# Kernel optimization log

Hardware: AMD Instinct MI355X
Metric: run time of the kernel (lower is better)

Reference implementation:

```python
import jax, jax.numpy as jnp
import numpy as np

PIXEL_THRESHOLD = 0.4
FRACTION_THRESHOLD = 0.03
NUM_CLASSES = 20
N, H, W = 100, 640, 960
LOGIT_SCALE = 8.0  # makes the instance-axis softmax peaky enough to cross PIXEL_THRESHOLD


def setup_inputs() -> dict:
    key = jax.random.key(0)
    k1, k2, k3 = jax.random.split(key, 3)
    cls_prob = jax.random.uniform(k1, (N,), dtype=jnp.float32)
    mask_prob = jax.random.normal(k2, (N, H, W), dtype=jnp.float32) * LOGIT_SCALE
    cls_idx = jax.random.randint(k3, (N,), 0, NUM_CLASSES)
    return {"cls_prob": cls_prob, "mask_prob": mask_prob, "cls_idx": cls_idx}


def _mask_removal(cls_prob, mask_prob, cls_idx):
    # Sort instances by class confidence, descending (greedy NMS order).
    order = jnp.argsort(-cls_prob)
    cls_prob_s = cls_prob[order]          # [N]
    cls_idx_s = cls_idx[order]            # [N]
    raw_s = mask_prob[order]              # [N,H,W] pre-softmax logits (mask_prob_copy)
    # Per-pixel softmax over the instance axis (permutation-equivariant, so
    # softmax-then-sort == sort-then-softmax as in the original).
    sm = jax.nn.softmax(raw_s, axis=0)    # [N,H,W]

    def step(state, inp):
        panoptic, mask_image = state      # [H,W], [C,H,W]
        smi, rawi, ci = inp
        logit = (smi >= PIXEL_THRESHOLD).astype(rawi.dtype)   # binarized mask [H,W]
        mask_sum = logit.sum()
        curr = mask_image[ci]
        overlap = jnp.sum((curr >= 1.0) & (logit == 1.0)).astype(rawi.dtype) / jnp.maximum(mask_sum, 1.0)
        degenerate = (logit.max() == logit.min()) | (mask_sum == 0.0)
        skip = degenerate | (overlap > FRACTION_THRESHOLD)
        # assign only unclaimed panoptic pixels inside the binarized mask
        assign = (panoptic == 0.0) & (logit == 1.0) & jnp.logical_not(skip)
        keep_mask = jnp.where(assign, rawi, 0.0)              # use_mask_low_constant=False
        panoptic = jnp.where(assign, 1.0, panoptic)
        mask_image = mask_image.at[ci].add(jnp.where(assign, logit, 0.0))
        return (panoptic, mask_image), (keep_mask, jnp.logical_not(skip))

    init = (jnp.zeros((H, W), jnp.float32), jnp.zeros((NUM_CLASSES, H, W), jnp.float32))
    _, (keep_masks, keep_flags) = jax.lax.scan(step, init, (sm, raw_s, cls_idx_s))
    # Fixed-shape outputs: keep_flags marks which (sorted) instances survived;
    # dropped instances have all-zero keep_masks rows.
    return cls_prob_s, keep_masks, cls_idx_s, keep_flags


def reference(cls_prob, mask_prob, cls_idx):
    return _mask_removal(cls_prob, mask_prob, cls_idx)
```

## Files before the change

### kernel.cpp

```cpp
#include <hip/hip_runtime.h>
#include <cstdint>
#include <cstddef>

#define N_INST 100
#define HW (640 * 960)
#define PIX_THR 0.4f
#define FRAC_THR 0.03f
#define EPS_BORDER 5e-5f
#define FLAG_CAP 65536
#define L2E 1.4426950408889634f

#define CB 1200
#define ZB 480
#define F4_TOTAL (N_INST * HW / 4)
#define F4_PER_BLOCK (F4_TOTAL / ZB)
#define F4_PER_THREAD (F4_PER_BLOCK / 128)

#define OUT_MASKS_OFF 100
#define OUT_CLSIDX_OFF (100 + (size_t)N_INST * HW)
#define OUT_FLAGS_OFF (100 + (size_t)N_INST * HW + N_INST)


__global__ __launch_bounds__(256) void k0_init(
    const float* __restrict__ cls_prob,
    const int* __restrict__ cls_idx,
    int* __restrict__ ord,
    int* __restrict__ rank_arr,
    float* __restrict__ out,
    unsigned* __restrict__ mask_sum,
    unsigned* __restrict__ flag_count,
    unsigned* __restrict__ pair_cnt) {
    int t = threadIdx.x;
    if (t < N_INST) {
        float pi = cls_prob[t];
        int rank = 0;
        for (int j = 0; j < N_INST; ++j) {
            float pj = cls_prob[j];
            rank += (pj > pi) || (pj == pi && j < t);
        }
        ord[rank] = t;
        rank_arr[t] = rank;
        out[rank] = pi;
        out[OUT_CLSIDX_OFF + rank] = (float)cls_idx[t];
        mask_sum[t] = 0u;
    }
    if (t == 0) *flag_count = 0u;
    for (int i = t; i < N_INST * N_INST; i += 256)
        pair_cnt[i] = 0u;
}

__global__ __launch_bounds__(128) void k1_fused(
    const float* __restrict__ mask,
    const int* __restrict__ rank_arr,
    unsigned* __restrict__ mask_sum,
    unsigned* __restrict__ pair_cnt,
    uint4* __restrict__ pvals,
    unsigned* __restrict__ flag_count,
    unsigned* __restrict__ flag_list,
    float* __restrict__ out) {
    int t = threadIdx.x;

    if (blockIdx.x >= CB) {
        int zb = blockIdx.x - CB;
        float4* dst = (float4*)(out + OUT_MASKS_OFF) + (size_t)zb * F4_PER_BLOCK + t;
        const float4 z4 = make_float4(0.0f, 0.0f, 0.0f, 0.0f);
#pragma unroll 10
        for (int k = 0; k < F4_PER_THREAD; ++k)
            dst[k * 128] = z4;
        return;
    }

    __shared__ int srank[N_INST];
    __shared__ unsigned ssum[N_INST];
    if (t < N_INST) {
        srank[t] = rank_arr[t];
        ssum[t] = 0u;
    }
    __syncthreads();

    int p0 = (blockIdx.x * 128 + t) * 4;
    const float* base = mask + p0;

    float S[4] = {0.0f, 0.0f, 0.0f, 0.0f};
    float m[4] = {-3.4e38f, -3.4e38f, -3.4e38f, -3.4e38f};
    float n[4] = {-3.4e38f, -3.4e38f, -3.4e38f, -3.4e38f};
    int ia[4] = {0, 0, 0, 0};
    int ib[4] = {0, 0, 0, 0};

#pragma unroll 10
    for (int i = 0; i < N_INST; ++i) {
        float4 v4 = *(const float4*)(base + (size_t)i * HW);
        float vv[4] = {v4.x, v4.y, v4.z, v4.w};
#pragma unroll
        for (int j = 0; j < 4; ++j) {
            float v = vv[j];
            S[j] += exp2f(v * L2E);
            bool gt = v > m[j];
            bool g2 = v > n[j];
            n[j] = fmaxf(n[j], fminf(m[j], v));
            ib[j] = gt ? ia[j] : (g2 ? i : ib[j]);
            ia[j] = gt ? i : ia[j];
            m[j] = fmaxf(m[j], v);
        }
    }

#pragma unroll
    for (int j = 0; j < 4; ++j) {
        int p = p0 + j;
        float e1 = exp2f(m[j] * L2E);
        float e2 = exp2f(n[j] * L2E);
        float t04 = 0.4f * S[j];
        float w = EPS_BORDER * S[j];
        bool q1 = e1 >= t04;
        bool border = (fabsf(e1 - t04) < w) || (q1 && fabsf(e2 - t04) < w);

        unsigned c = 0u;
        float vlo = 0.0f, vhi = 0.0f;
        if (border) {
            unsigned slot = atomicAdd(flag_count, 1u);
            if (slot < FLAG_CAP) flag_list[slot] = (unsigned)p;
        } else if (q1) {
            bool q2 = e2 >= t04;
            int r1 = srank[ia[j]];
            atomicAdd(&ssum[r1], 1u);
            if (q2) {
                int r2 = srank[ib[j]];
                atomicAdd(&ssum[r2], 1u);
                int lo = min(r1, r2), hi = max(r1, r2);
                atomicAdd(&pair_cnt[lo * N_INST + hi], 1u);
                c = (unsigned)(lo + 1) | ((unsigned)(hi + 1) << 8);
                vlo = (r1 < r2) ? m[j] : n[j];
                vhi = (r1 < r2) ? n[j] : m[j];
            } else {
                c = (unsigned)(r1 + 1);
                vlo = m[j];
            }
        }
        pvals[p] = make_uint4(c, __float_as_uint(vlo), __float_as_uint(vhi), 0u);
    }

    __syncthreads();
    if (t < N_INST && ssum[t] != 0u)
        atomicAdd(&mask_sum[t], ssum[t]);
}

__global__ void k1_repair(const float* __restrict__ mask,
                          const int* __restrict__ ord,
                          unsigned* __restrict__ mask_sum,
                          unsigned* __restrict__ pair_cnt,
                          uint4* __restrict__ pvals,
                          const unsigned* __restrict__ flag_count,
                          const unsigned* __restrict__ flag_list) {
    __shared__ int sord[N_INST];
    if (threadIdx.x < N_INST) sord[threadIdx.x] = ord[threadIdx.x];
    __syncthreads();

    unsigned nf = *flag_count;
    if (nf > FLAG_CAP) nf = FLAG_CAP;
    for (unsigned idx = blockIdx.x * blockDim.x + threadIdx.x; idx < nf;
         idx += gridDim.x * blockDim.x) {
        int p = (int)flag_list[idx];
        float v[N_INST];
#pragma unroll
        for (int i = 0; i < N_INST; ++i)
            v[i] = mask[(size_t)sord[i] * HW + p];

        float m = v[0];
        int p1 = 0;
        float m2 = -3.4e38f;
        int p2 = 0;
#pragma unroll
        for (int i = 1; i < N_INST; ++i) {
            if (v[i] > m) { m2 = m; p2 = p1; m = v[i]; p1 = i; }
            else if (v[i] > m2) { m2 = v[i]; p2 = i; }
        }
        float d = 0.0f;
#pragma unroll
        for (int i = 0; i < N_INST; ++i)
            d += expf(v[i] - m);

        float sm1 = 1.0f / d;
        float sm2 = expf(m2 - m) / d;
        bool q1 = (sm1 >= PIX_THR);
        bool q2 = (sm2 >= PIX_THR);
        unsigned c = 0u;
        float vlo = 0.0f, vhi = 0.0f;
        if (q1) {
            atomicAdd(&mask_sum[p1], 1u);
            if (q2) {
                atomicAdd(&mask_sum[p2], 1u);
                int lo = min(p1, p2), hi = max(p1, p2);
                atomicAdd(&pair_cnt[lo * N_INST + hi], 1u);
                c = (unsigned)(lo + 1) | ((unsigned)(hi + 1) << 8);
                vlo = v[lo];
                vhi = v[hi];
            } else {
                c = (unsigned)(p1 + 1);
                vlo = v[p1];
            }
        }
        pvals[p] = make_uint4(c, __float_as_uint(vlo), __float_as_uint(vhi), 0u);
    }
}

__global__ void k2_scan(const unsigned* __restrict__ mask_sum,
                        const unsigned* __restrict__ pair_cnt,
                        const int* __restrict__ ord,
                        const int* __restrict__ cls_idx,
                        int* __restrict__ keep,
                        float* __restrict__ out) {
    __shared__ unsigned spair[N_INST * N_INST];
    __shared__ int scls[N_INST];
    __shared__ unsigned sms[N_INST];
    __shared__ int skeep[N_INST];
    int t = threadIdx.x;
    for (int i = t; i < N_INST * N_INST; i += 256)
        spair[i] = pair_cnt[i];
    if (t < N_INST) {
        scls[t] = cls_idx[ord[t]];
        sms[t] = mask_sum[t];
    }
    __syncthreads();

    for (int b = 0; b < N_INST; ++b) {
        if (t < 64) {
            unsigned cnt = 0u;
            for (int a = t; a < b; a += 64)
                if (skeep[a] && scls[a] == scls[b])
                    cnt += spair[a * N_INST + b];
#pragma unroll
            for (int off = 32; off; off >>= 1)
                cnt += __shfl_down((int)cnt, off);
            if (t == 0) {
                unsigned ms = sms[b];
                float overlap = (float)cnt / fmaxf((float)ms, 1.0f);
                bool degen = (ms == 0u) || (ms == (unsigned)HW);
                bool skip = degen || (overlap > FRAC_THR);
                skeep[b] = skip ? 0 : 1;
            }
        }
        __syncthreads();
    }

    if (t < N_INST) {
        keep[t] = skeep[t];
        out[OUT_FLAGS_OFF + t] = (float)skeep[t];
    }
}

__global__ __launch_bounds__(256) void k3_scatter(
    const uint4* __restrict__ pvals,
    const int* __restrict__ keep,
    float* __restrict__ out) {
    __shared__ int skeep[N_INST];
    if (threadIdx.x < N_INST) skeep[threadIdx.x] = keep[threadIdx.x];
    __syncthreads();

    int p = blockIdx.x * 256 + threadIdx.x;
    uint4 pv = pvals[p];
    unsigned c = pv.x;
    if (c == 0u) return;
    int a = (int)(c & 0xFFu) - 1;
    int b = (int)(c >> 8) - 1;

    int inst;
    float val;
    if (skeep[a]) {
        inst = a;
        val = __uint_as_float(pv.y);
    } else if (b >= 0 && skeep[b]) {
        inst = b;
        val = __uint_as_float(pv.z);
    } else {
        return;
    }
    out[OUT_MASKS_OFF + (size_t)inst * HW + p] = val;
}

extern "C" void kernel_launch(void* const* d_in, const int* in_sizes, int n_in,
                              void* d_out, int out_size, void* d_ws, size_t ws_size,
                              hipStream_t stream) {
    const float* cls_prob = (const float*)d_in[0];
    const float* mask = (const float*)d_in[1];
    const int* cls_idx = (const int*)d_in[2];
    float* out = (float*)d_out;

    char* ws = (char*)d_ws;
    int* ord = (int*)(ws + 0);
    int* rank_arr = (int*)(ws + 512);
    int* keep = (int*)(ws + 1024);
    unsigned* mask_sum = (unsigned*)(ws + 1536);
    unsigned* flag_count = (unsigned*)(ws + 2048);
    unsigned* pair_cnt = (unsigned*)(ws + 4096);
    uint4* pvals = (uint4*)(ws + 65536);
    unsigned* flag_list = (unsigned*)(ws + 65536 + (size_t)HW * 16);

    k0_init<<<1, 256, 0, stream>>>(cls_prob, cls_idx, ord, rank_arr, out,
                                   mask_sum, flag_count, pair_cnt);
    k1_fused<<<CB + ZB, 128, 0, stream>>>(mask, rank_arr, mask_sum, pair_cnt,
                                          pvals, flag_count, flag_list, out);
    k1_repair<<<16, 256, 0, stream>>>(mask, ord, mask_sum, pair_cnt, pvals,
                                      flag_count, flag_list);
    k2_scan<<<1, 256, 0, stream>>>(mask_sum, pair_cnt, ord, cls_idx, keep, out);
    k3_scatter<<<HW / 256, 256, 0, stream>>>(pvals, keep, out);
}
```

Baseline: 248.5 us.

## Dynamically balance output zeroing across blocks and fuse repair with scan kernel

Zeroing of the large keep_masks output changes from a fixed per-block split to a work queue. Chunks are claimed through an atomic counter by every block, including compute blocks once they finish their softmax and top-two pass, so zero-fill stores can spread across the whole grid. The border-pixel repair kernel and the single-block greedy scan are merged into one launch: the last block to finish, found through an atomic done counter, runs the scan. This removes one kernel launch and its gap, but adds atomic contention and relies on threadfence for correctness.

```diff
diff --git a/kernel.cpp b/kernel.cpp
--- a/kernel.cpp
+++ b/kernel.cpp
@@ -11,10 +11,12 @@
 #define L2E 1.4426950408889634f
 
 #define CB 1200
-#define ZB 480
-#define F4_TOTAL (N_INST * HW / 4)
-#define F4_PER_BLOCK (F4_TOTAL / ZB)
-#define F4_PER_THREAD (F4_PER_BLOCK / 128)
+#define ZB 680
+#define GRID (CB + ZB)
+#define CHUNK_F4 15360
+#define CHUNK_ITER 120
+#define NCHUNK 1000
+#define FIN_BLOCKS 128
 
 #define OUT_MASKS_OFF 100
 #define OUT_CLSIDX_OFF (100 + (size_t)N_INST * HW)
@@ -28,7 +30,7 @@
     int* __restrict__ rank_arr,
     float* __restrict__ out,
     unsigned* __restrict__ mask_sum,
-    unsigned* __restrict__ flag_count,
+    unsigned* __restrict__ ctrs,
     unsigned* __restrict__ pair_cnt) {
     int t = threadIdx.x;
     if (t < N_INST) {
@@ -44,7 +46,7 @@
         out[OUT_CLSIDX_OFF + rank] = (float)cls_idx[t];
         mask_sum[t] = 0u;
     }
-    if (t == 0) *flag_count = 0u;
+    if (t < 3) ctrs[t] = 0u;
     for (int i = t; i < N_INST * N_INST; i += 256)
         pair_cnt[i] = 0u;
 }
@@ -57,108 +59,122 @@
     uint4* __restrict__ pvals,
     unsigned* __restrict__ flag_count,
     unsigned* __restrict__ flag_list,
+    unsigned* __restrict__ zctr,
     float* __restrict__ out) {
     int t = threadIdx.x;
-
-    if (blockIdx.x >= CB) {
-        int zb = blockIdx.x - CB;
-        float4* dst = (float4*)(out + OUT_MASKS_OFF) + (size_t)zb * F4_PER_BLOCK + t;
+    __shared__ unsigned s_chunk;
+
+    if (blockIdx.x < CB) {
+        __shared__ int srank[N_INST];
+        __shared__ unsigned ssum[N_INST];
+        if (t < N_INST) {
+            srank[t] = rank_arr[t];
+            ssum[t] = 0u;
+        }
+        __syncthreads();
+
+        int p0 = (blockIdx.x * 128 + t) * 4;
+        const float* base = mask + p0;
+
+        float S[4] = {0.0f, 0.0f, 0.0f, 0.0f};
+        float m[4] = {-3.4e38f, -3.4e38f, -3.4e38f, -3.4e38f};
+        float n[4] = {-3.4e38f, -3.4e38f, -3.4e38f, -3.4e38f};
+        int ia[4] = {0, 0, 0, 0};
+        int ib[4] = {0, 0, 0, 0};
+
+#pragma unroll 10
+        for (int i = 0; i < N_INST; ++i) {
+            float4 v4 = *(const float4*)(base + (size_t)i * HW);
+            float vv[4] = {v4.x, v4.y, v4.z, v4.w};
+#pragma unroll
+            for (int j = 0; j < 4; ++j) {
+                float v = vv[j];
+                S[j] += exp2f(v * L2E);
+                bool gt = v > m[j];
+                bool g2 = v > n[j];
+                n[j] = fmaxf(n[j], fminf(m[j], v));
+                ib[j] = gt ? ia[j] : (g2 ? i : ib[j]);
+                ia[j] = gt ? i : ia[j];
+                m[j] = fmaxf(m[j], v);
+            }
+        }
+
+#pragma unroll
+        for (int j = 0; j < 4; ++j) {
+            int p = p0 + j;
+            float e1 = exp2f(m[j] * L2E);
+            float e2 = exp2f(n[j] * L2E);
+            float t04 = 0.4f * S[j];
+            float w = EPS_BORDER * S[j];
+            bool q1 = e1 >= t04;
+            bool border = (fabsf(e1 - t04) < w) || (q1 && fabsf(e2 - t04) < w);
+
+            unsigned c = 0u;
+            float vlo = 0.0f, vhi = 0.0f;
+            if (border) {
+                unsigned slot = atomicAdd(flag_count, 1u);
+                if (slot < FLAG_CAP) flag_list[slot] = (unsigned)p;
+            } else if (q1) {
+                bool q2 = e2 >= t04;
+                int r1 = srank[ia[j]];
+                atomicAdd(&ssum[r1], 1u);
+                if (q2) {
+                    int r2 = srank[ib[j]];
+                    atomicAdd(&ssum[r2], 1u);
+                    int lo = min(r1, r2), hi = max(r1, r2);
+                    atomicAdd(&pair_cnt[lo * N_INST + hi], 1u);
+                    c = (unsigned)(lo + 1) | ((unsigned)(hi + 1) << 8);
+                    vlo = (r1 < r2) ? m[j] : n[j];
+                    vhi = (r1 < r2) ? n[j] : m[j];
+                } else {
+                    c = (unsigned)(r1 + 1);
+                    vlo = m[j];
+                }
+            }
+            pvals[p] = make_uint4(c, __float_as_uint(vlo), __float_as_uint(vhi), 0u);
+        }
+
+        __syncthreads();
+        if (t < N_INST && ssum[t] != 0u)
+            atomicAdd(&mask_sum[t], ssum[t]);
+    }
+
+    for (;;) {
+        if (t == 0) s_chunk = atomicAdd(zctr, 1u);
+        __syncthreads();
+        unsigned c = s_chunk;
+        __syncthreads();
+        if (c >= NCHUNK) break;
+        float4* dst = (float4*)(out + OUT_MASKS_OFF) + (size_t)c * CHUNK_F4 + t;
         const float4 z4 = make_float4(0.0f, 0.0f, 0.0f, 0.0f);
-#pragma unroll 10
-        for (int k = 0; k < F4_PER_THREAD; ++k)
+#pragma unroll 8
+        for (int k = 0; k < CHUNK_ITER; ++k)
             dst[k * 128] = z4;
-        return;
-    }
-
-    __shared__ int srank[N_INST];
-    __shared__ unsigned ssum[N_INST];
-    if (t < N_INST) {
-        srank[t] = rank_arr[t];
-        ssum[t] = 0u;
-    }
-    __syncthreads();
-
-    int p0 = (blockIdx.x * 128 + t) * 4;
-    const float* base = mask + p0;
-
-    float S[4] = {0.0f, 0.0f, 0.0f, 0.0f};
-    float m[4] = {-3.4e38f, -3.4e38f, -3.4e38f, -3.4e38f};
-    float n[4] = {-3.4e38f, -3.4e38f, -3.4e38f, -3.4e38f};
-    int ia[4] = {0, 0, 0, 0};
-    int ib[4] = {0, 0, 0, 0};
-
-#pragma unroll 10
-    for (int i = 0; i < N_INST; ++i) {
-        float4 v4 = *(const float4*)(base + (size_t)i * HW);
-        float vv[4] = {v4.x, v4.y, v4.z, v4.w};
-#pragma unroll
-        for (int j = 0; j < 4; ++j) {
-            float v = vv[j];
-            S[j] += exp2f(v * L2E);
-            bool gt = v > m[j];
-            bool g2 = v > n[j];
-            n[j] = fmaxf(n[j], fminf(m[j], v));
-            ib[j] = gt ? ia[j] : (g2 ? i : ib[j]);
-            ia[j] = gt ? i : ia[j];
-            m[j] = fmaxf(m[j], v);
-        }
-    }
-
-#pragma unroll
-    for (int j = 0; j < 4; ++j) {
-        int p = p0 + j;
-        float e1 = exp2f(m[j] * L2E);
-        float e2 = exp2f(n[j] * L2E);
-        float t04 = 0.4f * S[j];
-        float w = EPS_BORDER * S[j];
-        bool q1 = e1 >= t04;
-        bool border = (fabsf(e1 - t04) < w) || (q1 && fabsf(e2 - t04) < w);
-
-        unsigned c = 0u;
-        float vlo = 0.0f, vhi = 0.0f;
-        if (border) {
-            unsigned slot = atomicAdd(flag_count, 1u);
-            if (slot < FLAG_CAP) flag_list[slot] = (unsigned)p;
-        } else if (q1) {
-            bool q2 = e2 >= t04;
-            int r1 = srank[ia[j]];
-            atomicAdd(&ssum[r1], 1u);
-            if (q2) {
-                int r2 = srank[ib[j]];
-                atomicAdd(&ssum[r2], 1u);
-                int lo = min(r1, r2), hi = max(r1, r2);
-                atomicAdd(&pair_cnt[lo * N_INST + hi], 1u);
-                c = (unsigned)(lo + 1) | ((unsigned)(hi + 1) << 8);
-                vlo = (r1 < r2) ? m[j] : n[j];
-                vhi = (r1 < r2) ? n[j] : m[j];
-            } else {
-                c = (unsigned)(r1 + 1);
-                vlo = m[j];
-            }
-        }
-        pvals[p] = make_uint4(c, __float_as_uint(vlo), __float_as_uint(vhi), 0u);
-    }
-
-    __syncthreads();
-    if (t < N_INST && ssum[t] != 0u)
-        atomicAdd(&mask_sum[t], ssum[t]);
-}
-
-__global__ void k1_repair(const float* __restrict__ mask,
-                          const int* __restrict__ ord,
-                          unsigned* __restrict__ mask_sum,
-                          unsigned* __restrict__ pair_cnt,
-                          uint4* __restrict__ pvals,
-                          const unsigned* __restrict__ flag_count,
-                          const unsigned* __restrict__ flag_list) {
+    }
+}
+
+__global__ __launch_bounds__(256) void k2_finish(
+    const float* __restrict__ mask,
+    const int* __restrict__ ord,
+    const int* __restrict__ cls_idx,
+    unsigned* __restrict__ mask_sum,
+    unsigned* __restrict__ pair_cnt,
+    uint4* __restrict__ pvals,
+    const unsigned* __restrict__ flag_count,
+    const unsigned* __restrict__ flag_list,
+    unsigned* __restrict__ done,
+    int* __restrict__ keep,
+    float* __restrict__ out) {
     __shared__ int sord[N_INST];
-    if (threadIdx.x < N_INST) sord[threadIdx.x] = ord[threadIdx.x];
+    __shared__ unsigned s_last;
+    int t = threadIdx.x;
+    if (t < N_INST) sord[t] = ord[t];
     __syncthreads();
 
     unsigned nf = *flag_count;
     if (nf > FLAG_CAP) nf = FLAG_CAP;
-    for (unsigned idx = blockIdx.x * blockDim.x + threadIdx.x; idx < nf;
-         idx += gridDim.x * blockDim.x) {
+    for (unsigned idx = blockIdx.x * 256 + t; idx < nf;
+         idx += FIN_BLOCKS * 256) {
         int p = (int)flag_list[idx];
         float v[N_INST];
 #pragma unroll
@@ -201,23 +217,21 @@
         }
         pvals[p] = make_uint4(c, __float_as_uint(vlo), __float_as_uint(vhi), 0u);
     }
-}
-
-__global__ void k2_scan(const unsigned* __restrict__ mask_sum,
-                        const unsigned* __restrict__ pair_cnt,
-                        const int* __restrict__ ord,
-                        const int* __restrict__ cls_idx,
-                        int* __restrict__ keep,
-                        float* __restrict__ out) {
+
+    __threadfence();
+    if (t == 0) s_last = atomicAdd(done, 1u);
+    __syncthreads();
+    if (s_last != FIN_BLOCKS - 1) return;
+    __threadfence();
+
     __shared__ unsigned spair[N_INST * N_INST];
     __shared__ int scls[N_INST];
     __shared__ unsigned sms[N_INST];
     __shared__ int skeep[N_INST];
-    int t = threadIdx.x;
     for (int i = t; i < N_INST * N_INST; i += 256)
         spair[i] = pair_cnt[i];
     if (t < N_INST) {
-        scls[t] = cls_idx[ord[t]];
+        scls[t] = cls_idx[sord[t]];
         sms[t] = mask_sum[t];
     }
     __syncthreads();
@@ -290,17 +304,21 @@
     int* rank_arr = (int*)(ws + 512);
     int* keep = (int*)(ws + 1024);
     unsigned* mask_sum = (unsigned*)(ws + 1536);
-    unsigned* flag_count = (unsigned*)(ws + 2048);
+    unsigned* ctrs = (unsigned*)(ws + 2048);
     unsigned* pair_cnt = (unsigned*)(ws + 4096);
     uint4* pvals = (uint4*)(ws + 65536);
     unsigned* flag_list = (unsigned*)(ws + 65536 + (size_t)HW * 16);
 
+    unsigned* flag_count = &ctrs[0];
+    unsigned* zctr = &ctrs[1];
+    unsigned* done = &ctrs[2];
+
     k0_init<<<1, 256, 0, stream>>>(cls_prob, cls_idx, ord, rank_arr, out,
-                                   mask_sum, flag_count, pair_cnt);
-    k1_fused<<<CB + ZB, 128, 0, stream>>>(mask, rank_arr, mask_sum, pair_cnt,
-                                          pvals, flag_count, flag_list, out);
-    k1_repair<<<16, 256, 0, stream>>>(mask, ord, mask_sum, pair_cnt, pvals,
-                                      flag_count, flag_list);
-    k2_scan<<<1, 256, 0, stream>>>(mask_sum, pair_cnt, ord, cls_idx, keep, out);
+                                   mask_sum, ctrs, pair_cnt);
+    k1_fused<<<GRID, 128, 0, stream>>>(mask, rank_arr, mask_sum, pair_cnt,
+                                       pvals, flag_count, flag_list, zctr, out);
+    k2_finish<<<FIN_BLOCKS, 256, 0, stream>>>(mask, ord, cls_idx, mask_sum,
+                                              pair_cnt, pvals, flag_count,
+                                              flag_list, done, keep, out);
     k3_scatter<<<HW / 256, 256, 0, stream>>>(pvals, keep, out);
 }
```

Result: slower. 259.6 us (+4.5%).
